# Kernel tuning notes

Hardware: AMD Instinct MI355X
Metric: run time of the kernel (lower is better)

The kernel has to match this reference:

```python
import jax, jax.numpy as jnp
import numpy as np

EMBED_DIM = 256
UNITS = 512


def setup_inputs() -> dict:
    key = jax.random.key(0)
    ks = jax.random.split(key, 8)
    B, L = 2048, 64  # batch, 8*8 spatial locations
    features = jax.random.normal(ks[0], (B, L, EMBED_DIM), dtype=jnp.float32)
    hidden = jax.random.normal(ks[1], (B, UNITS), dtype=jnp.float32)
    s1 = 1.0 / np.sqrt(EMBED_DIM)
    s2 = 1.0 / np.sqrt(UNITS)
    W1 = jax.random.normal(ks[2], (EMBED_DIM, UNITS), dtype=jnp.float32) * s1
    b1 = jnp.zeros((UNITS,), dtype=jnp.float32)
    W2 = jax.random.normal(ks[3], (UNITS, UNITS), dtype=jnp.float32) * s2
    b2 = jnp.zeros((UNITS,), dtype=jnp.float32)
    V = jax.random.normal(ks[4], (UNITS, 1), dtype=jnp.float32) * s2
    bv = jnp.zeros((1,), dtype=jnp.float32)
    return {"features": features, "hidden": hidden, "W1": W1, "b1": b1,
            "W2": W2, "b2": b2, "V": V, "bv": bv}


def reference(features, hidden, W1, b1, W2, b2, V, bv):
    # features: [B, L, E], hidden: [B, U]
    # Bahdanau additive attention
    proj_f = jnp.einsum('ble,eu->blu', features, W1) + b1          # [B, L, U]
    proj_h = (hidden @ W2 + b2)[:, None, :]                        # [B, 1, U]
    e = jnp.tanh(proj_f + proj_h)                                  # [B, L, U]
    score = jnp.einsum('blu,uo->blo', e, V) + bv                   # [B, L, 1]
    attention_weights = jax.nn.softmax(score, axis=1)              # [B, L, 1]
    context_vector = jnp.sum(attention_weights * features, axis=1) # [B, E]
    return context_vector, attention_weights
```

## Files before the change

kernel.cpp:

```cpp
#include <hip/hip_runtime.h>
#include <math.h>

#define BATCH 2048
#define LDIM 64
#define EDIM 256
#define UDIM 512

typedef __attribute__((ext_vector_type(8))) _Float16 half8;
typedef __attribute__((ext_vector_type(4))) float floatx4;

__device__ inline float tanh_fast(float x) {
    float t = __builtin_amdgcn_exp2f(x * 2.88539008177792681f);
    return 1.f - 2.f * __builtin_amdgcn_rcpf(t + 1.f);
}
__device__ inline half8 cvt8(float4 f0, float4 f1) {
    half8 h;
    h[0] = (_Float16)f0.x; h[1] = (_Float16)f0.y;
    h[2] = (_Float16)f0.z; h[3] = (_Float16)f0.w;
    h[4] = (_Float16)f1.x; h[5] = (_Float16)f1.y;
    h[6] = (_Float16)f1.z; h[7] = (_Float16)f1.w;
    return h;
}
__device__ inline const half8* bfrag(const unsigned short* F, int kc, int ntg, int l) {
    return (const half8*)(F + ((((size_t)kc * 32 + ntg) * 64 + l) << 3));
}

__global__ __launch_bounds__(256) void prep_frag(const float* __restrict__ W1,
                                                 const float* __restrict__ W2,
                                                 unsigned short* __restrict__ F1,
                                                 unsigned short* __restrict__ F2) {
    __shared__ float S[32 * 128];
    int bid = blockIdx.x;
    const float* W; unsigned short* F; int kc, grp;
    if (bid < 32) { W = W1; F = F1; kc = bid >> 2; grp = bid & 3; }
    else { bid -= 32; W = W2; F = F2; kc = bid >> 2; grp = bid & 3; }
    const int tid = threadIdx.x;
    const float* src = W + (size_t)kc * 32 * UDIM + grp * 128;
    float4* Sv = (float4*)S;
#pragma unroll
    for (int i = 0; i < 4; ++i) {
        int f = tid + i * 256;
        int k = f >> 5, c4 = f & 31;
        Sv[f] = *(const float4*)(src + (size_t)k * UDIM + c4 * 4);
    }
    __syncthreads();
#pragma unroll
    for (int i = 0; i < 2; ++i) {
        int u = tid + i * 256;
        int lane = u & 63, ntl = u >> 6;
        int n_loc = ntl * 16 + (lane & 15);
        int k0 = (lane >> 4) * 8;
        half8 h;
#pragma unroll
        for (int j = 0; j < 8; ++j)
            h[j] = (_Float16)S[(k0 + j) * 128 + n_loc];
        int ntg = grp * 8 + ntl;
        *(half8*)(F + (((size_t)kc * 32 + ntg) * 64 + lane) * 8) = h;
    }
}

__global__ __launch_bounds__(256) void prep_ph(const float* __restrict__ hidden,
                                               const unsigned short* __restrict__ F2,
                                               const float* __restrict__ b1,
                                               const float* __restrict__ b2,
                                               float* __restrict__ ph) {
    const int tid = threadIdx.x;
    const int w = tid >> 6;
    const int l = tid & 63;
    const int r0 = blockIdx.x * 16;

    floatx4 acc[8];
#pragma unroll
    for (int i = 0; i < 8; ++i) acc[i] = (floatx4){0.f, 0.f, 0.f, 0.f};

    const float* ap = hidden + (size_t)(r0 + (l & 15)) * UDIM + ((l >> 4) << 3);

    float4 a0 = *(const float4*)(ap);
    float4 a1 = *(const float4*)(ap + 4);
    half8 B[8];
#pragma unroll
    for (int nt = 0; nt < 8; ++nt) B[nt] = *bfrag(F2, 0, w * 8 + nt, l);

    for (int kc = 0; kc < 16; ++kc) {
        half8 a = cvt8(a0, a1);
        float4 n0, n1; half8 NB[8];
        if (kc < 15) {
            n0 = *(const float4*)(ap + (kc + 1) * 32);
            n1 = *(const float4*)(ap + (kc + 1) * 32 + 4);
#pragma unroll
            for (int nt = 0; nt < 8; ++nt) NB[nt] = *bfrag(F2, kc + 1, w * 8 + nt, l);
        }
#pragma unroll
        for (int nt = 0; nt < 8; ++nt)
            acc[nt] = __builtin_amdgcn_mfma_f32_16x16x32_f16(a, B[nt], acc[nt], 0, 0, 0);
        if (kc < 15) {
            a0 = n0; a1 = n1;
#pragma unroll
            for (int nt = 0; nt < 8; ++nt) B[nt] = NB[nt];
        }
    }
#pragma unroll
    for (int nt = 0; nt < 8; ++nt) {
        const int n = (w * 8 + nt) * 16 + (l & 15);
        const float bias = b1[n] + b2[n];
#pragma unroll
        for (int r = 0; r < 4; ++r) {
            const int m = (l >> 4) * 4 + r;
            ph[(size_t)(r0 + m) * UDIM + n] = acc[nt][r] + bias;
        }
    }
}

__global__ __launch_bounds__(512, 4) void attn_main(
    const float* __restrict__ feat, const unsigned short* __restrict__ F1,
    const float* __restrict__ ph, const float* __restrict__ Vw,
    const float* __restrict__ bv,
    float* __restrict__ ctx_out, float* __restrict__ w_out)
{
    __shared__ unsigned short lA[8 * 4 * 64 * 8];
    __shared__ float phl[512];
    __shared__ float Vl[512];
    __shared__ float scp[8][64];
    __shared__ float wsm[64];
    __shared__ float ctxp[2][256];

    const int tid = threadIdx.x;
    const int w = tid >> 6;
    const int l = tid & 63;
    const size_t b = blockIdx.x;
    const float* fb = feat + b * (LDIM * EDIM);

    float4 f4[2][4];
#pragma unroll
    for (int p = 0; p < 2; ++p) {
        const int u = tid + 512 * p;
        const float4* gp = (const float4*)(fb + (u >> 4) * EDIM + (u & 15) * 16);
        f4[p][0] = gp[0]; f4[p][1] = gp[1]; f4[p][2] = gp[2]; f4[p][3] = gp[3];
    }
    phl[tid] = ph[b * UDIM + tid];
    Vl[tid]  = Vw[tid];

#pragma unroll
    for (int p = 0; p < 2; ++p) {
        const int u  = tid + 512 * p;
        const int r  = u >> 4, kc = (u & 15) >> 1, o = (u & 1) * 2;
        const int mt = r >> 4, rr = r & 15;
        const int base = (kc * 4 + mt) * 64;
        *(half8*)&lA[(base + ((o * 16 + rr) ^ kc)) * 8]       = cvt8(f4[p][0], f4[p][1]);
        *(half8*)&lA[(base + (((o + 1) * 16 + rr) ^ kc)) * 8] = cvt8(f4[p][2], f4[p][3]);
    }

    floatx4 acc[4][4];
#pragma unroll
    for (int i = 0; i < 4; ++i)
#pragma unroll
        for (int j = 0; j < 4; ++j) acc[i][j] = (floatx4){0.f, 0.f, 0.f, 0.f};

    __syncthreads();

    for (int kc = 0; kc < 8; ++kc) {
        half8 Bc[4];
#pragma unroll
        for (int nt = 0; nt < 4; ++nt) Bc[nt] = *bfrag(F1, kc, w * 4 + nt, l);
        half8 a[4];
#pragma unroll
        for (int mt = 0; mt < 4; ++mt)
            a[mt] = *(const half8*)&lA[((kc * 4 + mt) * 64 + (l ^ kc)) * 8];
#pragma unroll
        for (int nt = 0; nt < 4; ++nt)
#pragma unroll
            for (int mt = 0; mt < 4; ++mt)
                acc[nt][mt] = __builtin_amdgcn_mfma_f32_16x16x32_f16(
                    a[mt], Bc[nt], acc[nt][mt], 0, 0, 0);
    }

    float sv[4][4];
#pragma unroll
    for (int mt = 0; mt < 4; ++mt)
#pragma unroll
        for (int r = 0; r < 4; ++r) sv[mt][r] = 0.f;
#pragma unroll
    for (int nt = 0; nt < 4; ++nt) {
        const int n = (w * 4 + nt) * 16 + (l & 15);
        const float phn = phl[n];
        const float vn  = Vl[n];
#pragma unroll
        for (int mt = 0; mt < 4; ++mt)
#pragma unroll
            for (int r = 0; r < 4; ++r)
                sv[mt][r] += tanh_fast(acc[nt][mt][r] + phn) * vn;
    }
#pragma unroll
    for (int mt = 0; mt < 4; ++mt)
#pragma unroll
        for (int r = 0; r < 4; ++r) {
            float v = sv[mt][r];
            v += __shfl_xor(v, 1);
            v += __shfl_xor(v, 2);
            v += __shfl_xor(v, 4);
            v += __shfl_xor(v, 8);
            if ((l & 15) == 0) scp[w][mt * 16 + (l >> 4) * 4 + r] = v;
        }
    __syncthreads();

    if (tid < 64) {
        float s = bv[0];
#pragma unroll
        for (int wv = 0; wv < 8; ++wv) s += scp[wv][tid];
        float m = s;
        m = fmaxf(m, __shfl_xor(m, 32));
        m = fmaxf(m, __shfl_xor(m, 16));
        m = fmaxf(m, __shfl_xor(m, 8));
        m = fmaxf(m, __shfl_xor(m, 4));
        m = fmaxf(m, __shfl_xor(m, 2));
        m = fmaxf(m, __shfl_xor(m, 1));
        float e = __builtin_amdgcn_exp2f((s - m) * 1.44269504088896341f);
        float sum = e;
        sum += __shfl_xor(sum, 32);
        sum += __shfl_xor(sum, 16);
        sum += __shfl_xor(sum, 8);
        sum += __shfl_xor(sum, 4);
        sum += __shfl_xor(sum, 2);
        sum += __shfl_xor(sum, 1);
        float wgt = e / sum;
        wsm[tid] = wgt;
        w_out[b * LDIM + tid] = wgt;
    }
    __syncthreads();

    {
        const int e = tid & 255, h = tid >> 8;
        float c = 0.f;
#pragma unroll 8
        for (int ll = h * 32; ll < h * 32 + 32; ++ll)
            c = fmaf(wsm[ll], fb[ll * EDIM + e], c);
        ctxp[h][e] = c;
    }
    __syncthreads();
    if (tid < 256)
        ctx_out[b * EDIM + tid] = ctxp[0][tid] + ctxp[1][tid];
}

extern "C" void kernel_launch(void* const* d_in, const int* in_sizes, int n_in,
                              void* d_out, int out_size, void* d_ws, size_t ws_size,
                              hipStream_t stream) {
    const float* features = (const float*)d_in[0];
    const float* hidden   = (const float*)d_in[1];
    const float* W1       = (const float*)d_in[2];
    const float* b1       = (const float*)d_in[3];
    const float* W2       = (const float*)d_in[4];
    const float* b2       = (const float*)d_in[5];
    const float* Vw       = (const float*)d_in[6];
    const float* bv       = (const float*)d_in[7];

    float* ctx_out = (float*)d_out;
    float* w_out   = (float*)d_out + (size_t)BATCH * EDIM;

    float* ph = (float*)d_ws;
    unsigned short* F1 = (unsigned short*)(ph + (size_t)BATCH * UDIM);
    unsigned short* F2 = F1 + (size_t)8 * 32 * 64 * 8;

    prep_frag<<<dim3(96), dim3(256), 0, stream>>>(W1, W2, F1, F2);
    prep_ph<<<dim3(128), dim3(256), 0, stream>>>(hidden, F2, b1, b2, ph);
    attn_main<<<dim3(BATCH), dim3(512), 0, stream>>>(
        features, F1, ph, Vw, bv, ctx_out, w_out);
}
```

Before: 257.5 us.

## Fuse hidden projection into attention kernel and process 8 batches per block

Removes the separate prep_ph launch and its global round-trip of the hidden projection. Each 1024-thread block now computes the hidden projection for 8 batch rows in LDS, then loops over those rows. The next row's features are prefetched into a double-buffered LDS tile while the current row's scores and context are computed. This cuts the grid to 256 large blocks with more shared memory each, so occupancy and latency hiding may drop. Per-iteration barriers may also serialise work.

```diff
diff --git a/kernel.cpp b/kernel.cpp
--- a/kernel.cpp
+++ b/kernel.cpp
@@ -5,6 +5,8 @@
 #define LDIM 64
 #define EDIM 256
 #define UDIM 512
+#define G 8
+#define HLP 516
 
 typedef __attribute__((ext_vector_type(8))) _Float16 half8;
 typedef __attribute__((ext_vector_type(4))) float floatx4;
@@ -59,186 +61,182 @@
     }
 }
 
-__global__ __launch_bounds__(256) void prep_ph(const float* __restrict__ hidden,
-                                               const unsigned short* __restrict__ F2,
-                                               const float* __restrict__ b1,
-                                               const float* __restrict__ b2,
-                                               float* __restrict__ ph) {
+__global__ __launch_bounds__(1024, 4) void attn_main(
+    const float* __restrict__ feat, const unsigned short* __restrict__ F1,
+    const unsigned short* __restrict__ F2, const float* __restrict__ hidden,
+    const float* __restrict__ b1, const float* __restrict__ b2,
+    const float* __restrict__ Vw, const float* __restrict__ bv,
+    float* __restrict__ ctx_out, float* __restrict__ w_out)
+{
+    __shared__ _Float16 lA[2][16384];
+    __shared__ float hl[8 * HLP];
+    __shared__ float ph_all[G][UDIM];
+    __shared__ float Vl[UDIM];
+    __shared__ float scp[16][64];
+    __shared__ float wsm[64];
+    __shared__ float ctxp[4][256];
+
     const int tid = threadIdx.x;
     const int w = tid >> 6;
     const int l = tid & 63;
-    const int r0 = blockIdx.x * 16;
-
-    floatx4 acc[8];
-#pragma unroll
-    for (int i = 0; i < 8; ++i) acc[i] = (floatx4){0.f, 0.f, 0.f, 0.f};
-
-    const float* ap = hidden + (size_t)(r0 + (l & 15)) * UDIM + ((l >> 4) << 3);
-
-    float4 a0 = *(const float4*)(ap);
-    float4 a1 = *(const float4*)(ap + 4);
-    half8 B[8];
-#pragma unroll
-    for (int nt = 0; nt < 8; ++nt) B[nt] = *bfrag(F2, 0, w * 8 + nt, l);
-
-    for (int kc = 0; kc < 16; ++kc) {
-        half8 a = cvt8(a0, a1);
-        float4 n0, n1; half8 NB[8];
-        if (kc < 15) {
-            n0 = *(const float4*)(ap + (kc + 1) * 32);
-            n1 = *(const float4*)(ap + (kc + 1) * 32 + 4);
-#pragma unroll
-            for (int nt = 0; nt < 8; ++nt) NB[nt] = *bfrag(F2, kc + 1, w * 8 + nt, l);
-        }
-#pragma unroll
-        for (int nt = 0; nt < 8; ++nt)
-            acc[nt] = __builtin_amdgcn_mfma_f32_16x16x32_f16(a, B[nt], acc[nt], 0, 0, 0);
-        if (kc < 15) {
-            a0 = n0; a1 = n1;
-#pragma unroll
-            for (int nt = 0; nt < 8; ++nt) B[nt] = NB[nt];
-        }
-    }
-#pragma unroll
-    for (int nt = 0; nt < 8; ++nt) {
-        const int n = (w * 8 + nt) * 16 + (l & 15);
-        const float bias = b1[n] + b2[n];
-#pragma unroll
-        for (int r = 0; r < 4; ++r) {
-            const int m = (l >> 4) * 4 + r;
-            ph[(size_t)(r0 + m) * UDIM + n] = acc[nt][r] + bias;
-        }
-    }
-}
-
-__global__ __launch_bounds__(512, 4) void attn_main(
-    const float* __restrict__ feat, const unsigned short* __restrict__ F1,
-    const float* __restrict__ ph, const float* __restrict__ Vw,
-    const float* __restrict__ bv,
-    float* __restrict__ ctx_out, float* __restrict__ w_out)
-{
-    __shared__ unsigned short lA[8 * 4 * 64 * 8];
-    __shared__ float phl[512];
-    __shared__ float Vl[512];
-    __shared__ float scp[8][64];
-    __shared__ float wsm[64];
-    __shared__ float ctxp[2][256];
-
-    const int tid = threadIdx.x;
-    const int w = tid >> 6;
-    const int l = tid & 63;
-    const size_t b = blockIdx.x;
-    const float* fb = feat + b * (LDIM * EDIM);
-
-    float4 f4[2][4];
-#pragma unroll
-    for (int p = 0; p < 2; ++p) {
-        const int u = tid + 512 * p;
-        const float4* gp = (const float4*)(fb + (u >> 4) * EDIM + (u & 15) * 16);
-        f4[p][0] = gp[0]; f4[p][1] = gp[1]; f4[p][2] = gp[2]; f4[p][3] = gp[3];
-    }
-    phl[tid] = ph[b * UDIM + tid];
-    Vl[tid]  = Vw[tid];
-
-#pragma unroll
-    for (int p = 0; p < 2; ++p) {
-        const int u  = tid + 512 * p;
-        const int r  = u >> 4, kc = (u & 15) >> 1, o = (u & 1) * 2;
-        const int mt = r >> 4, rr = r & 15;
-        const int base = (kc * 4 + mt) * 64;
-        *(half8*)&lA[(base + ((o * 16 + rr) ^ kc)) * 8]       = cvt8(f4[p][0], f4[p][1]);
-        *(half8*)&lA[(base + (((o + 1) * 16 + rr) ^ kc)) * 8] = cvt8(f4[p][2], f4[p][3]);
-    }
-
-    floatx4 acc[4][4];
-#pragma unroll
-    for (int i = 0; i < 4; ++i)
-#pragma unroll
-        for (int j = 0; j < 4; ++j) acc[i][j] = (floatx4){0.f, 0.f, 0.f, 0.f};
-
+    const size_t b0 = (size_t)blockIdx.x * G;
+
+    const int ar = tid >> 4, ac = (tid & 15) * 16;
+    const int skc = (tid & 15) >> 1, so = (tid & 1) * 2;
+    const int smt = ar >> 4, srr = ar & 15;
+
+    const float4* gp0 = (const float4*)(feat + b0 * (LDIM * EDIM) + ar * EDIM + ac);
+    float4 s0 = gp0[0], s1 = gp0[1], s2 = gp0[2], s3 = gp0[3];
+
+    {
+        int f = tid * 4, row = f >> 9, col = f & 511;
+        *(float4*)&hl[row * HLP + col] =
+            *(const float4*)(hidden + b0 * UDIM + f);
+    }
+    if (tid < 512) Vl[tid] = Vw[tid];
     __syncthreads();
 
-    for (int kc = 0; kc < 8; ++kc) {
-        half8 Bc[4];
-#pragma unroll
-        for (int nt = 0; nt < 4; ++nt) Bc[nt] = *bfrag(F1, kc, w * 4 + nt, l);
-        half8 a[4];
+    {
+        floatx4 pacc[2];
+        pacc[0] = (floatx4){0.f, 0.f, 0.f, 0.f};
+        pacc[1] = (floatx4){0.f, 0.f, 0.f, 0.f};
+        const float* hrow = hl + (l & 7) * HLP + ((l >> 4) << 3);
+#pragma unroll 2
+        for (int kc = 0; kc < 16; ++kc) {
+            float4 h0 = *(const float4*)(hrow + kc * 32);
+            float4 h1 = *(const float4*)(hrow + kc * 32 + 4);
+            half8 a = cvt8(h0, h1);
+#pragma unroll
+            for (int nt = 0; nt < 2; ++nt) {
+                half8 bf = *bfrag(F2, kc, w * 2 + nt, l);
+                pacc[nt] = __builtin_amdgcn_mfma_f32_16x16x32_f16(a, bf, pacc[nt], 0, 0, 0);
+            }
+        }
+#pragma unroll
+        for (int nt = 0; nt < 2; ++nt) {
+            const int n = (w * 2 + nt) * 16 + (l & 15);
+            const float bias = b1[n] + b2[n];
+            if ((l >> 4) < 2) {
+#pragma unroll
+                for (int r = 0; r < 4; ++r)
+                    ph_all[(l >> 4) * 4 + r][n] = pacc[nt][r] + bias;
+            }
+        }
+    }
+    {
+        _Float16* dst = &lA[0][((skc * 4 + smt) * 64) * 8];
+        *(half8*)(dst + (((so * 16 + srr) ^ skc)) * 8)       = cvt8(s0, s1);
+        *(half8*)(dst + ((((so + 1) * 16 + srr) ^ skc)) * 8) = cvt8(s2, s3);
+    }
+    __syncthreads();
+
+    const float bvv = bv[0];
+
+    for (int g = 0; g < G; ++g) {
+        const int cur = g & 1;
+        const size_t b = b0 + g;
+        const float* fb = feat + b * (LDIM * EDIM);
+
+        float4 p0, p1, p2, p3;
+        if (g < G - 1) {
+            const float4* gp = (const float4*)(fb + LDIM * EDIM + ar * EDIM + ac);
+            p0 = gp[0]; p1 = gp[1]; p2 = gp[2]; p3 = gp[3];
+        }
+
+        floatx4 acc[2][4];
+#pragma unroll
+        for (int i = 0; i < 2; ++i)
+#pragma unroll
+            for (int j = 0; j < 4; ++j) acc[i][j] = (floatx4){0.f, 0.f, 0.f, 0.f};
+#pragma unroll
+        for (int kc = 0; kc < 8; ++kc) {
+            half8 B0 = *bfrag(F1, kc, w * 2 + 0, l);
+            half8 B1 = *bfrag(F1, kc, w * 2 + 1, l);
+            half8 a[4];
+#pragma unroll
+            for (int mt = 0; mt < 4; ++mt)
+                a[mt] = *(const half8*)&lA[cur][((kc * 4 + mt) * 64 + (l ^ kc)) * 8];
+#pragma unroll
+            for (int mt = 0; mt < 4; ++mt) {
+                acc[0][mt] = __builtin_amdgcn_mfma_f32_16x16x32_f16(a[mt], B0, acc[0][mt], 0, 0, 0);
+                acc[1][mt] = __builtin_amdgcn_mfma_f32_16x16x32_f16(a[mt], B1, acc[1][mt], 0, 0, 0);
+            }
+        }
+
+        float sv[4][4];
 #pragma unroll
         for (int mt = 0; mt < 4; ++mt)
-            a[mt] = *(const half8*)&lA[((kc * 4 + mt) * 64 + (l ^ kc)) * 8];
-#pragma unroll
-        for (int nt = 0; nt < 4; ++nt)
+#pragma unroll
+            for (int r = 0; r < 4; ++r) sv[mt][r] = 0.f;
+#pragma unroll
+        for (int nt = 0; nt < 2; ++nt) {
+            const int n = (w * 2 + nt) * 16 + (l & 15);
+            const float phn = ph_all[g][n];
+            const float vn  = Vl[n];
 #pragma unroll
             for (int mt = 0; mt < 4; ++mt)
-                acc[nt][mt] = __builtin_amdgcn_mfma_f32_16x16x32_f16(
-                    a[mt], Bc[nt], acc[nt][mt], 0, 0, 0);
-    }
-
-    float sv[4][4];
-#pragma unroll
-    for (int mt = 0; mt < 4; ++mt)
-#pragma unroll
-        for (int r = 0; r < 4; ++r) sv[mt][r] = 0.f;
-#pragma unroll
-    for (int nt = 0; nt < 4; ++nt) {
-        const int n = (w * 4 + nt) * 16 + (l & 15);
-        const float phn = phl[n];
-        const float vn  = Vl[n];
+#pragma unroll
+                for (int r = 0; r < 4; ++r)
+                    sv[mt][r] += tanh_fast(acc[nt][mt][r] + phn) * vn;
+        }
 #pragma unroll
         for (int mt = 0; mt < 4; ++mt)
 #pragma unroll
-            for (int r = 0; r < 4; ++r)
-                sv[mt][r] += tanh_fast(acc[nt][mt][r] + phn) * vn;
-    }
-#pragma unroll
-    for (int mt = 0; mt < 4; ++mt)
-#pragma unroll
-        for (int r = 0; r < 4; ++r) {
-            float v = sv[mt][r];
-            v += __shfl_xor(v, 1);
-            v += __shfl_xor(v, 2);
-            v += __shfl_xor(v, 4);
-            v += __shfl_xor(v, 8);
-            if ((l & 15) == 0) scp[w][mt * 16 + (l >> 4) * 4 + r] = v;
-        }
-    __syncthreads();
-
-    if (tid < 64) {
-        float s = bv[0];
-#pragma unroll
-        for (int wv = 0; wv < 8; ++wv) s += scp[wv][tid];
-        float m = s;
-        m = fmaxf(m, __shfl_xor(m, 32));
-        m = fmaxf(m, __shfl_xor(m, 16));
-        m = fmaxf(m, __shfl_xor(m, 8));
-        m = fmaxf(m, __shfl_xor(m, 4));
-        m = fmaxf(m, __shfl_xor(m, 2));
-        m = fmaxf(m, __shfl_xor(m, 1));
-        float e = __builtin_amdgcn_exp2f((s - m) * 1.44269504088896341f);
-        float sum = e;
-        sum += __shfl_xor(sum, 32);
-        sum += __shfl_xor(sum, 16);
-        sum += __shfl_xor(sum, 8);
-        sum += __shfl_xor(sum, 4);
-        sum += __shfl_xor(sum, 2);
-        sum += __shfl_xor(sum, 1);
-        float wgt = e / sum;
-        wsm[tid] = wgt;
-        w_out[b * LDIM + tid] = wgt;
-    }
-    __syncthreads();
-
-    {
-        const int e = tid & 255, h = tid >> 8;
-        float c = 0.f;
-#pragma unroll 8
-        for (int ll = h * 32; ll < h * 32 + 32; ++ll)
-            c = fmaf(wsm[ll], fb[ll * EDIM + e], c);
-        ctxp[h][e] = c;
-    }
-    __syncthreads();
-    if (tid < 256)
-        ctx_out[b * EDIM + tid] = ctxp[0][tid] + ctxp[1][tid];
+            for (int r = 0; r < 4; ++r) {
+                float v = sv[mt][r];
+                v += __shfl_xor(v, 1);
+                v += __shfl_xor(v, 2);
+                v += __shfl_xor(v, 4);
+                v += __shfl_xor(v, 8);
+                if ((l & 15) == 0) scp[w][mt * 16 + (l >> 4) * 4 + r] = v;
+            }
+        __syncthreads();
+
+        if (tid < 64) {
+            float s = bvv;
+#pragma unroll
+            for (int wv = 0; wv < 16; ++wv) s += scp[wv][tid];
+            float m = s;
+            m = fmaxf(m, __shfl_xor(m, 32));
+            m = fmaxf(m, __shfl_xor(m, 16));
+            m = fmaxf(m, __shfl_xor(m, 8));
+            m = fmaxf(m, __shfl_xor(m, 4));
+            m = fmaxf(m, __shfl_xor(m, 2));
+            m = fmaxf(m, __shfl_xor(m, 1));
+            float e = __builtin_amdgcn_exp2f((s - m) * 1.44269504088896341f);
+            float sum = e;
+            sum += __shfl_xor(sum, 32);
+            sum += __shfl_xor(sum, 16);
+            sum += __shfl_xor(sum, 8);
+            sum += __shfl_xor(sum, 4);
+            sum += __shfl_xor(sum, 2);
+            sum += __shfl_xor(sum, 1);
+            float wgt = e / sum;
+            wsm[tid] = wgt;
+            w_out[b * LDIM + tid] = wgt;
+        }
+        __syncthreads();
+
+        {
+            const int h = tid >> 8, e = tid & 255;
+            const float* fr = fb + (h * 16) * EDIM + e;
+            float c = 0.f;
+#pragma unroll
+            for (int i = 0; i < 16; ++i)
+                c = fmaf(wsm[h * 16 + i], fr[i * EDIM], c);
+            ctxp[h][e] = c;
+        }
+        if (g < G - 1) {
+            _Float16* dst = &lA[cur ^ 1][((skc * 4 + smt) * 64) * 8];
+            *(half8*)(dst + (((so * 16 + srr) ^ skc)) * 8)       = cvt8(p0, p1);
+            *(half8*)(dst + ((((so + 1) * 16 + srr) ^ skc)) * 8) = cvt8(p2, p3);
+        }
+        __syncthreads();
+
+        if (tid < 256)
+            ctx_out[b * EDIM + tid] =
+                ctxp[0][tid] + ctxp[1][tid] + ctxp[2][tid] + ctxp[3][tid];
+    }
 }
 
 extern "C" void kernel_launch(void* const* d_in, const int* in_sizes, int n_in,
@@ -256,12 +254,10 @@
     float* ctx_out = (float*)d_out;
     float* w_out   = (float*)d_out + (size_t)BATCH * EDIM;
 
-    float* ph = (float*)d_ws;
-    unsigned short* F1 = (unsigned short*)(ph + (size_t)BATCH * UDIM);
+    unsigned short* F1 = (unsigned short*)d_ws;
     unsigned short* F2 = F1 + (size_t)8 * 32 * 64 * 8;
 
     prep_frag<<<dim3(96), dim3(256), 0, stream>>>(W1, W2, F1, F2);
-    prep_ph<<<dim3(128), dim3(256), 0, stream>>>(hidden, F2, b1, b2, ph);
-    attn_main<<<dim3(BATCH), dim3(512), 0, stream>>>(
-        features, F1, ph, Vw, bv, ctx_out, w_out);
-}
+    attn_main<<<dim3(BATCH / G), dim3(1024), 0, stream>>>(
+        features, F1, F2, hidden, b1, b2, Vw, bv, ctx_out, w_out);
+}
```

After: 322.0 us. 25.0% more time.
